# Kernel optimization log

Hardware: AMD Instinct MI355X
Metric: run time of the kernel (lower is better)

The kernel has to match this reference:

```python
import jax, jax.numpy as jnp
import numpy as np

EPS = 1e-12  # torch F.normalize eps
NEG = -9999.0  # masked_fill value from the source


def _l2norm(x):
    n = jnp.linalg.norm(x, axis=-1, keepdims=True)
    return x / jnp.maximum(n, EPS)


def _maxsim(q, d, mask_f, mask_b):
    # q: [B,Lq,D]; d: [N,B,Ld,D]; mask: [N,B,Ld]
    rep = _l2norm(d * mask_f[..., None])
    s = jnp.einsum('bqd,nbkd->nbqk', q, rep)  # [N,B,Lq,Ld]
    s = jnp.where(mask_b[:, :, None, :], s, NEG)
    return s.max(axis=-1).sum(axis=-1)  # [N,B]


def setup_inputs() -> dict:
    key = jax.random.key(0)
    k0, k1, k2, k3, k4 = jax.random.split(key, 5)
    B, N, Lq, Ld, D = 128, 8, 32, 256, 128
    return {
        'q_reps': jax.random.normal(k0, (B, Lq, D), jnp.float32),
        'd_cq': jax.random.normal(k1, (N, B, Ld, D), jnp.float32),
        'd_orig': jax.random.normal(k2, (N, B, Ld, D), jnp.float32),
        'd_mask': jax.random.randint(k3, (N, B, Ld), 0, 2).astype(jnp.int32),
        'labels': jax.random.normal(k4, (B, N), jnp.float32),
    }


def reference(q_reps, d_cq, d_orig, d_mask, labels):
    # teacher='default', loss_type='kldiv' path
    q = _l2norm(q_reps)  # normalize query tokens over D
    mask_f = d_mask.astype(q_reps.dtype)
    mask_b = d_mask.astype(bool)
    scores = _maxsim(q, d_cq, mask_f, mask_b).T        # [B,N] student (cq) MaxSim
    scores_label = _maxsim(q, d_orig, mask_f, mask_b).T  # [B,N] teacher (orig) MaxSim
    # softmax->log in the source == log_softmax (same math, stable form)
    log_s = jax.nn.log_softmax(scores, axis=-1)
    log_t = jax.nn.log_softmax(scores_label, axis=-1)
    # KLDivLoss(reduction='batchmean', log_target=True)
    B = scores.shape[0]
    loss = jnp.sum(jnp.exp(log_t) * (log_t - log_s)) / B
    return loss
```

## Files before the change

### kernel.cpp

```cpp
#include <hip/hip_runtime.h>
#include <math.h>

#define Bq 128
#define Nn 8
#define LQ 32
#define LD 256
#define DD 128
#define EPSN 1e-12f
#define NEGV (-9999.0f)

typedef __attribute__((ext_vector_type(8))) short short8v;
typedef __attribute__((ext_vector_type(4))) int   int4v;
typedef __attribute__((ext_vector_type(4))) float f32x4;

__device__ __forceinline__ unsigned bf16_rne_hibits(float x) {
    unsigned u = __float_as_uint(x);
    return (u + 0x7FFFu + ((u >> 16) & 1u)) & 0xFFFF0000u;
}

__global__ __launch_bounds__(256) void qnorm_k(const float* __restrict__ q,
                                               unsigned short* __restrict__ qh,
                                               unsigned short* __restrict__ ql) {
    int row  = blockIdx.x * 4 + (threadIdx.x >> 6);
    int lane = threadIdx.x & 63;
    size_t base = (size_t)row * DD + lane * 2;
    float2 v = *reinterpret_cast<const float2*>(q + base);
    float ss = v.x * v.x + v.y * v.y;
#pragma unroll
    for (int o = 32; o; o >>= 1) ss += __shfl_xor(ss, o);
    float inv = 1.0f / fmaxf(sqrtf(ss), EPSN);
    float x0 = v.x * inv, x1 = v.y * inv;
    unsigned h0 = bf16_rne_hibits(x0), h1 = bf16_rne_hibits(x1);
    float l0 = x0 - __uint_as_float(h0);
    float l1 = x1 - __uint_as_float(h1);
    unsigned g0 = bf16_rne_hibits(l0), g1 = bf16_rne_hibits(l1);
    *reinterpret_cast<unsigned*>(qh + base) = (h0 >> 16) | h1;
    *reinterpret_cast<unsigned*>(ql + base) = (g0 >> 16) | g1;
}

__global__ __launch_bounds__(256) void maxsim_k(const float* __restrict__ d_cq,
                                                const float* __restrict__ d_orig,
                                                const int* __restrict__ mask,
                                                const unsigned short* __restrict__ qh,
                                                const unsigned short* __restrict__ ql,
                                                float* __restrict__ scores) {
    __shared__ float wm[4][32];

    int bid = blockIdx.x;
    int tau = bid >> 10;
    int nb  = bid & 1023;
    int b   = nb & 127;
    int n   = nb >> 7;

    int tid  = threadIdx.x;
    int w    = tid >> 6;
    int lane = tid & 63;
    int r    = lane & 15;
    int g    = lane >> 4;

    const float* dbase = (tau ? d_orig : d_cq) + (size_t)nb * (LD * DD);

    const unsigned short* qh_r = qh + ((size_t)b * LQ + r) * DD + g * 8;
    const unsigned short* ql_r = ql + ((size_t)b * LQ + r) * DD + g * 8;

    f32x4 rm0 = {NEGV, NEGV, NEGV, NEGV};
    f32x4 rm1 = {NEGV, NEGV, NEGV, NEGV};

#define SB __builtin_amdgcn_sched_barrier(0)

#define CVT2(W, X0, X1)                                                        \
    { unsigned h0 = bf16_rne_hibits(X0), h1 = bf16_rne_hibits(X1);             \
      float lf0 = (X0) - __uint_as_float(h0);                                  \
      float lf1 = (X1) - __uint_as_float(h1);                                  \
      dhw[W] = (int)((h0 >> 16) | h1);                                         \
      dlw[W] = (int)((bf16_rne_hibits(lf0) >> 16) | bf16_rne_hibits(lf1));     \
      ssq += (X0)*(X0) + (X1)*(X1); }

#define KSTEP(C0, C1, KS, PFOFF)                                               \
    {                                                                          \
        short8v a0h = *reinterpret_cast<const short8v*>(qh_r  + (KS) * 32);    \
        short8v a0l = *reinterpret_cast<const short8v*>(ql_r  + (KS) * 32);    \
        short8v a1h = *reinterpret_cast<const short8v*>(qh_r + 16 * DD + (KS) * 32); \
        short8v a1l = *reinterpret_cast<const short8v*>(ql_r + 16 * DD + (KS) * 32); \
        int4v dhw, dlw;                                                        \
        CVT2(0, C0.x, C0.y) CVT2(1, C0.z, C0.w)                                \
        CVT2(2, C1.x, C1.y) CVT2(3, C1.z, C1.w)                                \
        C0 = *reinterpret_cast<const float4*>(prow + (PFOFF));                 \
        C1 = *reinterpret_cast<const float4*>(prow + (PFOFF) + 4);             \
        short8v dh = __builtin_bit_cast(short8v, dhw);                         \
        short8v dl = __builtin_bit_cast(short8v, dlw);                         \
        c0 = __builtin_amdgcn_mfma_f32_16x16x32_bf16(a0h, dh, c0, 0, 0, 0);    \
        c1 = __builtin_amdgcn_mfma_f32_16x16x32_bf16(a1h, dh, c1, 0, 0, 0);    \
        c0 = __builtin_amdgcn_mfma_f32_16x16x32_bf16(a0h, dl, c0, 0, 0, 0);    \
        c1 = __builtin_amdgcn_mfma_f32_16x16x32_bf16(a1h, dl, c1, 0, 0, 0);    \
        c0 = __builtin_amdgcn_mfma_f32_16x16x32_bf16(a0l, dh, c0, 0, 0, 0);    \
        c1 = __builtin_amdgcn_mfma_f32_16x16x32_bf16(a1l, dh, c1, 0, 0, 0);    \
    }

    const float* prow = dbase + (size_t)(w * 64 + r) * DD + g * 8;
    float4 A0 = *reinterpret_cast<const float4*>(prow);
    float4 A1 = *reinterpret_cast<const float4*>(prow + 4);
    float4 B0 = *reinterpret_cast<const float4*>(prow + 32);
    float4 B1 = *reinterpret_cast<const float4*>(prow + 36);

#pragma unroll 1
    for (int nt = 0; nt < 4; ++nt) {
        int drow = w * 64 + nt * 16 + r;

        f32x4 c0 = {0.f, 0.f, 0.f, 0.f};
        f32x4 c1 = {0.f, 0.f, 0.f, 0.f};
        float ssq = 0.0f;

        int mk = mask[(size_t)nb * LD + drow];
        int nnoff = (nt < 3) ? 2048 : 0;

        KSTEP(A0, A1, 0, 64);          SB;
        KSTEP(B0, B1, 1, 96);          SB;
        KSTEP(A0, A1, 2, nnoff);       SB;
        KSTEP(B0, B1, 3, nnoff + 32);  SB;

        ssq += __shfl_xor(ssq, 16);
        ssq += __shfl_xor(ssq, 32);
        float inv = 1.0f / fmaxf(sqrtf(ssq), EPSN);

#pragma unroll
        for (int i = 0; i < 4; ++i) {
            float s0 = mk ? c0[i] * inv : NEGV;
            float s1 = mk ? c1[i] * inv : NEGV;
            rm0[i] = fmaxf(rm0[i], s0);
            rm1[i] = fmaxf(rm1[i], s1);
        }
        prow += 16 * DD;
    }
#undef KSTEP
#undef CVT2

#pragma unroll
    for (int i = 0; i < 4; ++i) {
#pragma unroll
        for (int o = 1; o <= 8; o <<= 1) {
            rm0[i] = fmaxf(rm0[i], __shfl_xor(rm0[i], o));
            rm1[i] = fmaxf(rm1[i], __shfl_xor(rm1[i], o));
        }
    }
    if (r == 0) {
#pragma unroll
        for (int i = 0; i < 4; ++i) {
            wm[w][g * 4 + i]      = rm0[i];
            wm[w][16 + g * 4 + i] = rm1[i];
        }
    }
    __syncthreads();

    if (tid < 32) {
        float v = fmaxf(fmaxf(wm[0][tid], wm[1][tid]),
                        fmaxf(wm[2][tid], wm[3][tid]));
#pragma unroll
        for (int o = 1; o <= 16; o <<= 1) v += __shfl_xor(v, o);
        if (tid == 0)
            scores[tau * (Bq * Nn) + b * Nn + n] = v;
    }
}

__global__ void loss_k(const float* __restrict__ scores, float* __restrict__ out) {
    int tid = threadIdx.x;
    const float* s = scores + tid * Nn;
    const float* t = scores + Bq * Nn + tid * Nn;
    float sv[Nn], tv[Nn];
#pragma unroll
    for (int n = 0; n < Nn; ++n) { sv[n] = s[n]; tv[n] = t[n]; }
    float ms = sv[0], mt = tv[0];
#pragma unroll
    for (int n = 1; n < Nn; ++n) { ms = fmaxf(ms, sv[n]); mt = fmaxf(mt, tv[n]); }
    float es = 0.0f, et = 0.0f;
#pragma unroll
    for (int n = 0; n < Nn; ++n) { es += expf(sv[n] - ms); et += expf(tv[n] - mt); }
    float lses = ms + logf(es);
    float lset = mt + logf(et);
    double kl = 0.0;
#pragma unroll
    for (int n = 0; n < Nn; ++n) {
        float lt = tv[n] - lset;
        float ls = sv[n] - lses;
        kl += (double)expf(lt) * ((double)lt - (double)ls);
    }
#pragma unroll
    for (int o = 32; o; o >>= 1) kl += __shfl_xor(kl, o);
    __shared__ double part[2];
    if ((tid & 63) == 0) part[tid >> 6] = kl;
    __syncthreads();
    if (tid == 0) out[0] = (float)((part[0] + part[1]) / (double)Bq);
}

extern "C" void kernel_launch(void* const* d_in, const int* in_sizes, int n_in,
                              void* d_out, int out_size, void* d_ws, size_t ws_size,
                              hipStream_t stream) {
    const float* q     = (const float*)d_in[0];
    const float* dcq   = (const float*)d_in[1];
    const float* dorig = (const float*)d_in[2];
    const int*   mask  = (const int*)d_in[3];

    unsigned short* qh = (unsigned short*)d_ws;
    unsigned short* ql = qh + (size_t)Bq * LQ * DD;
    float* scores      = (float*)(ql + (size_t)Bq * LQ * DD);

    qnorm_k<<<(Bq * LQ) / 4, 256, 0, stream>>>(q, qh, ql);
    maxsim_k<<<2 * Nn * Bq, 256, 0, stream>>>(dcq, dorig, mask, qh, ql, scores);
    loss_k<<<1, 128, 0, stream>>>(scores, (float*)d_out);
}
```

Measured before the change: 69.26 us.

## Process student and teacher documents in one block to share query loads and mask

Each block now handles both d_cq and d_orig for the same (n,b) pair instead of launching separate blocks per tensor. Query fragments, the mask and the loop overhead are shared across the two computations, and two independent MFMA chains and loads are interleaved to raise instruction-level parallelism. The cost is half as many blocks (1024), roughly double the live registers per thread, and possibly lower occupancy.

```diff
diff --git a/kernel.cpp b/kernel.cpp
--- a/kernel.cpp
+++ b/kernel.cpp
@@ -44,13 +44,12 @@
                                                 const unsigned short* __restrict__ qh,
                                                 const unsigned short* __restrict__ ql,
                                                 float* __restrict__ scores) {
-    __shared__ float wm[4][32];
-
-    int bid = blockIdx.x;
-    int tau = bid >> 10;
-    int nb  = bid & 1023;
-    int b   = nb & 127;
-    int n   = nb >> 7;
+    __shared__ float wma[4][32];
+    __shared__ float wmb[4][32];
+
+    int nb = blockIdx.x;
+    int b  = nb & 127;
+    int n  = nb >> 7;
 
     int tid  = threadIdx.x;
     int w    = tid >> 6;
@@ -58,79 +57,101 @@
     int r    = lane & 15;
     int g    = lane >> 4;
 
-    const float* dbase = (tau ? d_orig : d_cq) + (size_t)nb * (LD * DD);
-
     const unsigned short* qh_r = qh + ((size_t)b * LQ + r) * DD + g * 8;
     const unsigned short* ql_r = ql + ((size_t)b * LQ + r) * DD + g * 8;
 
-    f32x4 rm0 = {NEGV, NEGV, NEGV, NEGV};
-    f32x4 rm1 = {NEGV, NEGV, NEGV, NEGV};
+    f32x4 rm0a = {NEGV, NEGV, NEGV, NEGV}, rm1a = {NEGV, NEGV, NEGV, NEGV};
+    f32x4 rm0b = {NEGV, NEGV, NEGV, NEGV}, rm1b = {NEGV, NEGV, NEGV, NEGV};
 
 #define SB __builtin_amdgcn_sched_barrier(0)
 
-#define CVT2(W, X0, X1)                                                        \
+#define CVT2(DH, DL, W, X0, X1, SSQ)                                           \
     { unsigned h0 = bf16_rne_hibits(X0), h1 = bf16_rne_hibits(X1);             \
       float lf0 = (X0) - __uint_as_float(h0);                                  \
       float lf1 = (X1) - __uint_as_float(h1);                                  \
-      dhw[W] = (int)((h0 >> 16) | h1);                                         \
-      dlw[W] = (int)((bf16_rne_hibits(lf0) >> 16) | bf16_rne_hibits(lf1));     \
-      ssq += (X0)*(X0) + (X1)*(X1); }
-
-#define KSTEP(C0, C1, KS, PFOFF)                                               \
+      DH[W] = (int)((h0 >> 16) | h1);                                          \
+      DL[W] = (int)((bf16_rne_hibits(lf0) >> 16) | bf16_rne_hibits(lf1));      \
+      SSQ += (X0)*(X0) + (X1)*(X1); }
+
+#define KSTEP(CA0, CA1, CB0, CB1, KS, PFOFF)                                   \
     {                                                                          \
-        short8v a0h = *reinterpret_cast<const short8v*>(qh_r  + (KS) * 32);    \
-        short8v a0l = *reinterpret_cast<const short8v*>(ql_r  + (KS) * 32);    \
+        short8v a0h = *reinterpret_cast<const short8v*>(qh_r + (KS) * 32);     \
+        short8v a0l = *reinterpret_cast<const short8v*>(ql_r + (KS) * 32);     \
         short8v a1h = *reinterpret_cast<const short8v*>(qh_r + 16 * DD + (KS) * 32); \
         short8v a1l = *reinterpret_cast<const short8v*>(ql_r + 16 * DD + (KS) * 32); \
-        int4v dhw, dlw;                                                        \
-        CVT2(0, C0.x, C0.y) CVT2(1, C0.z, C0.w)                                \
-        CVT2(2, C1.x, C1.y) CVT2(3, C1.z, C1.w)                                \
-        C0 = *reinterpret_cast<const float4*>(prow + (PFOFF));                 \
-        C1 = *reinterpret_cast<const float4*>(prow + (PFOFF) + 4);             \
-        short8v dh = __builtin_bit_cast(short8v, dhw);                         \
-        short8v dl = __builtin_bit_cast(short8v, dlw);                         \
-        c0 = __builtin_amdgcn_mfma_f32_16x16x32_bf16(a0h, dh, c0, 0, 0, 0);    \
-        c1 = __builtin_amdgcn_mfma_f32_16x16x32_bf16(a1h, dh, c1, 0, 0, 0);    \
-        c0 = __builtin_amdgcn_mfma_f32_16x16x32_bf16(a0h, dl, c0, 0, 0, 0);    \
-        c1 = __builtin_amdgcn_mfma_f32_16x16x32_bf16(a1h, dl, c1, 0, 0, 0);    \
-        c0 = __builtin_amdgcn_mfma_f32_16x16x32_bf16(a0l, dh, c0, 0, 0, 0);    \
-        c1 = __builtin_amdgcn_mfma_f32_16x16x32_bf16(a1l, dh, c1, 0, 0, 0);    \
-    }
-
-    const float* prow = dbase + (size_t)(w * 64 + r) * DD + g * 8;
-    float4 A0 = *reinterpret_cast<const float4*>(prow);
-    float4 A1 = *reinterpret_cast<const float4*>(prow + 4);
-    float4 B0 = *reinterpret_cast<const float4*>(prow + 32);
-    float4 B1 = *reinterpret_cast<const float4*>(prow + 36);
+        int4v dhwa, dlwa, dhwb, dlwb;                                          \
+        CVT2(dhwa, dlwa, 0, CA0.x, CA0.y, ssqa)                                \
+        CVT2(dhwa, dlwa, 1, CA0.z, CA0.w, ssqa)                                \
+        CVT2(dhwa, dlwa, 2, CA1.x, CA1.y, ssqa)                                \
+        CVT2(dhwa, dlwa, 3, CA1.z, CA1.w, ssqa)                                \
+        CA0 = *reinterpret_cast<const float4*>(prow_a + (PFOFF));              \
+        CA1 = *reinterpret_cast<const float4*>(prow_a + (PFOFF) + 4);          \
+        CVT2(dhwb, dlwb, 0, CB0.x, CB0.y, ssqb)                                \
+        CVT2(dhwb, dlwb, 1, CB0.z, CB0.w, ssqb)                                \
+        CVT2(dhwb, dlwb, 2, CB1.x, CB1.y, ssqb)                                \
+        CVT2(dhwb, dlwb, 3, CB1.z, CB1.w, ssqb)                                \
+        CB0 = *reinterpret_cast<const float4*>(prow_b + (PFOFF));              \
+        CB1 = *reinterpret_cast<const float4*>(prow_b + (PFOFF) + 4);          \
+        short8v dha = __builtin_bit_cast(short8v, dhwa);                       \
+        short8v dla = __builtin_bit_cast(short8v, dlwa);                       \
+        c0a = __builtin_amdgcn_mfma_f32_16x16x32_bf16(a0h, dha, c0a, 0, 0, 0); \
+        c1a = __builtin_amdgcn_mfma_f32_16x16x32_bf16(a1h, dha, c1a, 0, 0, 0); \
+        c0a = __builtin_amdgcn_mfma_f32_16x16x32_bf16(a0h, dla, c0a, 0, 0, 0); \
+        c1a = __builtin_amdgcn_mfma_f32_16x16x32_bf16(a1h, dla, c1a, 0, 0, 0); \
+        c0a = __builtin_amdgcn_mfma_f32_16x16x32_bf16(a0l, dha, c0a, 0, 0, 0); \
+        c1a = __builtin_amdgcn_mfma_f32_16x16x32_bf16(a1l, dha, c1a, 0, 0, 0); \
+        short8v dhb = __builtin_bit_cast(short8v, dhwb);                       \
+        short8v dlb = __builtin_bit_cast(short8v, dlwb);                       \
+        c0b = __builtin_amdgcn_mfma_f32_16x16x32_bf16(a0h, dhb, c0b, 0, 0, 0); \
+        c1b = __builtin_amdgcn_mfma_f32_16x16x32_bf16(a1h, dhb, c1b, 0, 0, 0); \
+        c0b = __builtin_amdgcn_mfma_f32_16x16x32_bf16(a0h, dlb, c0b, 0, 0, 0); \
+        c1b = __builtin_amdgcn_mfma_f32_16x16x32_bf16(a1h, dlb, c1b, 0, 0, 0); \
+        c0b = __builtin_amdgcn_mfma_f32_16x16x32_bf16(a0l, dhb, c0b, 0, 0, 0); \
+        c1b = __builtin_amdgcn_mfma_f32_16x16x32_bf16(a1l, dhb, c1b, 0, 0, 0); \
+    }
+
+    const float* prow_a = d_cq   + (size_t)nb * (LD * DD) + (size_t)(w * 64 + r) * DD + g * 8;
+    const float* prow_b = d_orig + (size_t)nb * (LD * DD) + (size_t)(w * 64 + r) * DD + g * 8;
+
+    float4 Xa0 = *reinterpret_cast<const float4*>(prow_a);
+    float4 Xa1 = *reinterpret_cast<const float4*>(prow_a + 4);
+    float4 Xb0 = *reinterpret_cast<const float4*>(prow_b);
+    float4 Xb1 = *reinterpret_cast<const float4*>(prow_b + 4);
+    float4 Ya0 = *reinterpret_cast<const float4*>(prow_a + 32);
+    float4 Ya1 = *reinterpret_cast<const float4*>(prow_a + 36);
+    float4 Yb0 = *reinterpret_cast<const float4*>(prow_b + 32);
+    float4 Yb1 = *reinterpret_cast<const float4*>(prow_b + 36);
 
 #pragma unroll 1
     for (int nt = 0; nt < 4; ++nt) {
         int drow = w * 64 + nt * 16 + r;
 
-        f32x4 c0 = {0.f, 0.f, 0.f, 0.f};
-        f32x4 c1 = {0.f, 0.f, 0.f, 0.f};
-        float ssq = 0.0f;
+        f32x4 c0a = {0.f, 0.f, 0.f, 0.f}, c1a = {0.f, 0.f, 0.f, 0.f};
+        f32x4 c0b = {0.f, 0.f, 0.f, 0.f}, c1b = {0.f, 0.f, 0.f, 0.f};
+        float ssqa = 0.0f, ssqb = 0.0f;
 
         int mk = mask[(size_t)nb * LD + drow];
         int nnoff = (nt < 3) ? 2048 : 0;
 
-        KSTEP(A0, A1, 0, 64);          SB;
-        KSTEP(B0, B1, 1, 96);          SB;
-        KSTEP(A0, A1, 2, nnoff);       SB;
-        KSTEP(B0, B1, 3, nnoff + 32);  SB;
-
-        ssq += __shfl_xor(ssq, 16);
-        ssq += __shfl_xor(ssq, 32);
-        float inv = 1.0f / fmaxf(sqrtf(ssq), EPSN);
+        KSTEP(Xa0, Xa1, Xb0, Xb1, 0, 64);         SB;
+        KSTEP(Ya0, Ya1, Yb0, Yb1, 1, 96);         SB;
+        KSTEP(Xa0, Xa1, Xb0, Xb1, 2, nnoff);      SB;
+        KSTEP(Ya0, Ya1, Yb0, Yb1, 3, nnoff + 32); SB;
+
+        ssqa += __shfl_xor(ssqa, 16);  ssqa += __shfl_xor(ssqa, 32);
+        ssqb += __shfl_xor(ssqb, 16);  ssqb += __shfl_xor(ssqb, 32);
+        float inva = 1.0f / fmaxf(sqrtf(ssqa), EPSN);
+        float invb = 1.0f / fmaxf(sqrtf(ssqb), EPSN);
 
 #pragma unroll
         for (int i = 0; i < 4; ++i) {
-            float s0 = mk ? c0[i] * inv : NEGV;
-            float s1 = mk ? c1[i] * inv : NEGV;
-            rm0[i] = fmaxf(rm0[i], s0);
-            rm1[i] = fmaxf(rm1[i], s1);
+            rm0a[i] = fmaxf(rm0a[i], mk ? c0a[i] * inva : NEGV);
+            rm1a[i] = fmaxf(rm1a[i], mk ? c1a[i] * inva : NEGV);
+            rm0b[i] = fmaxf(rm0b[i], mk ? c0b[i] * invb : NEGV);
+            rm1b[i] = fmaxf(rm1b[i], mk ? c1b[i] * invb : NEGV);
         }
-        prow += 16 * DD;
+        prow_a += 16 * DD;
+        prow_b += 16 * DD;
     }
 #undef KSTEP
 #undef CVT2
@@ -139,25 +160,31 @@
     for (int i = 0; i < 4; ++i) {
 #pragma unroll
         for (int o = 1; o <= 8; o <<= 1) {
-            rm0[i] = fmaxf(rm0[i], __shfl_xor(rm0[i], o));
-            rm1[i] = fmaxf(rm1[i], __shfl_xor(rm1[i], o));
+            rm0a[i] = fmaxf(rm0a[i], __shfl_xor(rm0a[i], o));
+            rm1a[i] = fmaxf(rm1a[i], __shfl_xor(rm1a[i], o));
+            rm0b[i] = fmaxf(rm0b[i], __shfl_xor(rm0b[i], o));
+            rm1b[i] = fmaxf(rm1b[i], __shfl_xor(rm1b[i], o));
         }
     }
     if (r == 0) {
 #pragma unroll
         for (int i = 0; i < 4; ++i) {
-            wm[w][g * 4 + i]      = rm0[i];
-            wm[w][16 + g * 4 + i] = rm1[i];
+            wma[w][g * 4 + i]      = rm0a[i];
+            wma[w][16 + g * 4 + i] = rm1a[i];
+            wmb[w][g * 4 + i]      = rm0b[i];
+            wmb[w][16 + g * 4 + i] = rm1b[i];
         }
     }
     __syncthreads();
 
-    if (tid < 32) {
-        float v = fmaxf(fmaxf(wm[0][tid], wm[1][tid]),
-                        fmaxf(wm[2][tid], wm[3][tid]));
+    if (tid < 64) {
+        int tau = tid >> 5, l = tid & 31;
+        const float (*wm)[32] = tau ? wmb : wma;
+        float v = fmaxf(fmaxf(wm[0][l], wm[1][l]),
+                        fmaxf(wm[2][l], wm[3][l]));
 #pragma unroll
         for (int o = 1; o <= 16; o <<= 1) v += __shfl_xor(v, o);
-        if (tid == 0)
+        if (l == 0)
             scores[tau * (Bq * Nn) + b * Nn + n] = v;
     }
 }
@@ -205,6 +232,6 @@
     float* scores      = (float*)(ql + (size_t)Bq * LQ * DD);
 
     qnorm_k<<<(Bq * LQ) / 4, 256, 0, stream>>>(q, qh, ql);
-    maxsim_k<<<2 * Nn * Bq, 256, 0, stream>>>(dcq, dorig, mask, qh, ql, scores);
+    maxsim_k<<<Nn * Bq, 256, 0, stream>>>(dcq, dorig, mask, qh, ql, scores);
     loss_k<<<1, 128, 0, stream>>>(scores, (float*)d_out);
 }
```

Result: faster. 65.56 us (-5.3%).

## Stage swizzled query splits in LDS and truncate doc bf16 split

Applied to the files above, without the earlier changes.

Each block now stages the query's hi/lo bf16 fragments (16 KB) in shared memory, and the qnorm kernel writes them with an XOR swizzle so LDS reads avoid bank conflicts. This replaces the per-k-step global loads of the query fragments. The document bf16 hi/lo split now uses truncation instead of round-to-nearest, which cuts ALU work in the conversion loop but may slightly change precision. The MFMA order is regrouped so the second query half is loaded after the first three MFMAs, and the launch bounds request 8 blocks per CU.

```diff
diff --git a/kernel.cpp b/kernel.cpp
--- a/kernel.cpp
+++ b/kernel.cpp
@@ -34,16 +34,18 @@
     float l0 = x0 - __uint_as_float(h0);
     float l1 = x1 - __uint_as_float(h1);
     unsigned g0 = bf16_rne_hibits(l0), g1 = bf16_rne_hibits(l1);
-    *reinterpret_cast<unsigned*>(qh + base) = (h0 >> 16) | h1;
-    *reinterpret_cast<unsigned*>(ql + base) = (g0 >> 16) | g1;
-}
-
-__global__ __launch_bounds__(256) void maxsim_k(const float* __restrict__ d_cq,
-                                                const float* __restrict__ d_orig,
-                                                const int* __restrict__ mask,
-                                                const unsigned short* __restrict__ qh,
-                                                const unsigned short* __restrict__ ql,
-                                                float* __restrict__ scores) {
+    unsigned swz = ((unsigned)(lane * 2)) ^ (((unsigned)row & 7u) << 3);
+    *reinterpret_cast<unsigned*>(qh + (size_t)row * DD + swz) = (h0 >> 16) | h1;
+    *reinterpret_cast<unsigned*>(ql + (size_t)row * DD + swz) = (g0 >> 16) | g1;
+}
+
+__global__ __launch_bounds__(256, 8) void maxsim_k(const float* __restrict__ d_cq,
+                                                   const float* __restrict__ d_orig,
+                                                   const int* __restrict__ mask,
+                                                   const unsigned short* __restrict__ qh,
+                                                   const unsigned short* __restrict__ ql,
+                                                   float* __restrict__ scores) {
+    __shared__ float4 qstage[1024];
     __shared__ float wm[4][32];
 
     int bid = blockIdx.x;
@@ -58,10 +60,19 @@
     int r    = lane & 15;
     int g    = lane >> 4;
 
-    const float* dbase = (tau ? d_orig : d_cq) + (size_t)nb * (LD * DD);
-
-    const unsigned short* qh_r = qh + ((size_t)b * LQ + r) * DD + g * 8;
-    const unsigned short* ql_r = ql + ((size_t)b * LQ + r) * DD + g * 8;
+    {
+        const float4* srch = reinterpret_cast<const float4*>(qh + (size_t)b * LQ * DD);
+        const float4* srcl = reinterpret_cast<const float4*>(ql + (size_t)b * LQ * DD);
+        qstage[tid]       = srch[tid];
+        qstage[tid + 256] = srch[tid + 256];
+        qstage[tid + 512] = srcl[tid];
+        qstage[tid + 768] = srcl[tid + 256];
+    }
+    __syncthreads();
+
+    const unsigned short* qh_lds = reinterpret_cast<const unsigned short*>(qstage);
+    const unsigned short* ql_lds = qh_lds + LQ * DD;
+    unsigned swz8 = ((unsigned)r & 7u) << 3;
 
     f32x4 rm0 = {NEGV, NEGV, NEGV, NEGV};
     f32x4 rm1 = {NEGV, NEGV, NEGV, NEGV};
@@ -69,19 +80,16 @@
 #define SB __builtin_amdgcn_sched_barrier(0)
 
 #define CVT2(W, X0, X1)                                                        \
-    { unsigned h0 = bf16_rne_hibits(X0), h1 = bf16_rne_hibits(X1);             \
-      float lf0 = (X0) - __uint_as_float(h0);                                  \
-      float lf1 = (X1) - __uint_as_float(h1);                                  \
-      dhw[W] = (int)((h0 >> 16) | h1);                                         \
-      dlw[W] = (int)((bf16_rne_hibits(lf0) >> 16) | bf16_rne_hibits(lf1));     \
+    { unsigned u0 = __float_as_uint(X0), u1 = __float_as_uint(X1);             \
+      dhw[W] = (int)((u0 >> 16) | (u1 & 0xFFFF0000u));                         \
+      float l0 = (X0) - __uint_as_float(u0 & 0xFFFF0000u);                     \
+      float l1 = (X1) - __uint_as_float(u1 & 0xFFFF0000u);                     \
+      dlw[W] = (int)((__float_as_uint(l0) >> 16) |                             \
+                    (__float_as_uint(l1) & 0xFFFF0000u));                      \
       ssq += (X0)*(X0) + (X1)*(X1); }
 
 #define KSTEP(C0, C1, KS, PFOFF)                                               \
     {                                                                          \
-        short8v a0h = *reinterpret_cast<const short8v*>(qh_r  + (KS) * 32);    \
-        short8v a0l = *reinterpret_cast<const short8v*>(ql_r  + (KS) * 32);    \
-        short8v a1h = *reinterpret_cast<const short8v*>(qh_r + 16 * DD + (KS) * 32); \
-        short8v a1l = *reinterpret_cast<const short8v*>(ql_r + 16 * DD + (KS) * 32); \
         int4v dhw, dlw;                                                        \
         CVT2(0, C0.x, C0.y) CVT2(1, C0.z, C0.w)                                \
         CVT2(2, C1.x, C1.y) CVT2(3, C1.z, C1.w)                                \
@@ -89,19 +97,27 @@
         C1 = *reinterpret_cast<const float4*>(prow + (PFOFF) + 4);             \
         short8v dh = __builtin_bit_cast(short8v, dhw);                         \
         short8v dl = __builtin_bit_cast(short8v, dlw);                         \
+        unsigned aoff = (((unsigned)(KS) * 32u) + (unsigned)g * 8u) ^ swz8;    \
+        short8v a0h = *reinterpret_cast<const short8v*>(qh_lds + r * DD + aoff);        \
+        short8v a0l = *reinterpret_cast<const short8v*>(ql_lds + r * DD + aoff);        \
         c0 = __builtin_amdgcn_mfma_f32_16x16x32_bf16(a0h, dh, c0, 0, 0, 0);    \
+        c0 = __builtin_amdgcn_mfma_f32_16x16x32_bf16(a0h, dl, c0, 0, 0, 0);    \
+        c0 = __builtin_amdgcn_mfma_f32_16x16x32_bf16(a0l, dh, c0, 0, 0, 0);    \
+        SB;                                                                    \
+        short8v a1h = *reinterpret_cast<const short8v*>(qh_lds + (r + 16) * DD + aoff); \
+        short8v a1l = *reinterpret_cast<const short8v*>(ql_lds + (r + 16) * DD + aoff); \
         c1 = __builtin_amdgcn_mfma_f32_16x16x32_bf16(a1h, dh, c1, 0, 0, 0);    \
-        c0 = __builtin_amdgcn_mfma_f32_16x16x32_bf16(a0h, dl, c0, 0, 0, 0);    \
         c1 = __builtin_amdgcn_mfma_f32_16x16x32_bf16(a1h, dl, c1, 0, 0, 0);    \
-        c0 = __builtin_amdgcn_mfma_f32_16x16x32_bf16(a0l, dh, c0, 0, 0, 0);    \
         c1 = __builtin_amdgcn_mfma_f32_16x16x32_bf16(a1l, dh, c1, 0, 0, 0);    \
     }
 
-    const float* prow = dbase + (size_t)(w * 64 + r) * DD + g * 8;
-    float4 A0 = *reinterpret_cast<const float4*>(prow);
-    float4 A1 = *reinterpret_cast<const float4*>(prow + 4);
-    float4 B0 = *reinterpret_cast<const float4*>(prow + 32);
-    float4 B1 = *reinterpret_cast<const float4*>(prow + 36);
+    const float* prow = (tau ? d_orig : d_cq)
+        + (size_t)nb * (LD * DD) + (size_t)(w * 64 + r) * DD + g * 8;
+
+    float4 X0 = *reinterpret_cast<const float4*>(prow);
+    float4 X1 = *reinterpret_cast<const float4*>(prow + 4);
+    float4 Y0 = *reinterpret_cast<const float4*>(prow + 32);
+    float4 Y1 = *reinterpret_cast<const float4*>(prow + 36);
 
 #pragma unroll 1
     for (int nt = 0; nt < 4; ++nt) {
@@ -114,10 +130,10 @@
         int mk = mask[(size_t)nb * LD + drow];
         int nnoff = (nt < 3) ? 2048 : 0;
 
-        KSTEP(A0, A1, 0, 64);          SB;
-        KSTEP(B0, B1, 1, 96);          SB;
-        KSTEP(A0, A1, 2, nnoff);       SB;
-        KSTEP(B0, B1, 3, nnoff + 32);  SB;
+        KSTEP(X0, X1, 0, 64);          SB;
+        KSTEP(Y0, Y1, 1, 96);          SB;
+        KSTEP(X0, X1, 2, nnoff);       SB;
+        KSTEP(Y0, Y1, 3, nnoff + 32);  SB;
 
         ssq += __shfl_xor(ssq, 16);
         ssq += __shfl_xor(ssq, 32);
@@ -125,10 +141,8 @@
 
 #pragma unroll
         for (int i = 0; i < 4; ++i) {
-            float s0 = mk ? c0[i] * inv : NEGV;
-            float s1 = mk ? c1[i] * inv : NEGV;
-            rm0[i] = fmaxf(rm0[i], s0);
-            rm1[i] = fmaxf(rm1[i], s1);
+            rm0[i] = fmaxf(rm0[i], mk ? c0[i] * inv : NEGV);
+            rm1[i] = fmaxf(rm1[i], mk ? c1[i] * inv : NEGV);
         }
         prow += 16 * DD;
     }
```

Result: slower. 101.9 us (+47.1%).
